# Performance work log

Measured on AMD Instinct MI355X. Metric: run time of the kernel, lower is better.

Reference implementation:

```python
import jax, jax.numpy as jnp
import numpy as np

DIM = 256          # model dim
HK = 8             # kv heads
HQ = 32            # query heads
H = HQ // HK       # queries per kv group
DH = 128           # head dim (== DIM//2, required by RoPE assert)
B = 1
T = 2048
THETA = 10000.0
CACHE = 8192       # RoPE cached seq_len; module uses _freqs_cis[-T:]


def _rope(x):
    # x: [..., T, DH]; positions are the LAST T of the cached 8192 (faithful to _freqs_cis[-T:])
    t = x.shape[-2]
    half = DH  # == DIM // 2
    pos = jnp.arange(CACHE - t, CACHE, dtype=jnp.float32)
    inv_freq = THETA ** (-(jnp.arange(half, dtype=jnp.float32) / half))
    f = pos[:, None] * inv_freq[None, :]            # [T, DH]
    cos, sin = jnp.cos(f), jnp.sin(f)
    x1, x2 = jnp.split(x, 2, axis=-1)
    rot = jnp.concatenate((-x2, x1), axis=-1)       # rotate_half
    return x * cos + rot * sin


def setup_inputs() -> dict:
    key = jax.random.key(0)
    ks = jax.random.split(key, 7)
    q = jax.random.normal(ks[0], (B, T, DIM), jnp.float32)
    k = jax.random.normal(ks[1], (B, T, DIM), jnp.float32)
    v = jax.random.normal(ks[2], (B, T, DIM), jnp.float32)
    mask = jnp.tril(jnp.ones((T, T), dtype=bool))   # causal
    Wq = jax.random.normal(ks[3], (DIM, HQ * DH), jnp.float32) * 0.02
    Wk = jax.random.normal(ks[4], (DIM, HK * DH), jnp.float32) * 0.02
    Wv = jax.random.normal(ks[5], (DIM, HK * DH), jnp.float32) * 0.02
    Wo = jax.random.normal(ks[6], (HQ * DH, DIM), jnp.float32) * 0.02
    return {"q": q, "k": k, "v": v, "mask": mask, "Wq": Wq, "Wk": Wk, "Wv": Wv, "Wo": Wo}


def reference(q, k, v, mask, Wq, Wk, Wv, Wo):
    b, t, _ = q.shape
    # projections + head split; query heads grouped as (HK, H)
    qi = (q @ Wq).reshape(b, t, HQ, DH).transpose(0, 2, 1, 3).reshape(b, HK, H, t, DH)
    ki = (k @ Wk).reshape(b, t, HK, DH).transpose(0, 2, 1, 3)  # [b, HK, t, DH]
    vi = (v @ Wv).reshape(b, t, HK, DH).transpose(0, 2, 1, 3)  # [b, HK, t, DH]
    # RoPE on q, k AND v (module applies _apply_rope to all three)
    qi = _rope(qi)
    ki = _rope(ki)
    vi = _rope(vi)
    s = jnp.einsum('bghid,bgjd->bghij', qi, ki) / jnp.sqrt(jnp.asarray(DH, qi.dtype))
    neg = -jnp.finfo(s.dtype).max
    s = jnp.where(mask, s, neg)
    attn = jax.nn.softmax(s, axis=-1)               # [b, HK, H, t, t]
    vals = jnp.einsum('bghij,bgjd->bghid', attn, vi)
    vals = vals.transpose(0, 3, 1, 2, 4).reshape(b, t, HQ * DH)
    return vals @ Wo
```

## Files before the change

### kernel.cpp

```cpp
#include <hip/hip_runtime.h>
#include <hip/hip_bf16.h>
#include <math.h>

#define TSEQ 2048
#define NHQ 32
#define NHK 8
#define DH 128

typedef __attribute__((ext_vector_type(8))) short short8;
typedef __attribute__((ext_vector_type(4))) float f32x4;
typedef __attribute__((ext_vector_type(4))) short s16x4;

__device__ __forceinline__ short f2bf(float f) {
  union { float f; unsigned u; } v; v.f = f;
  unsigned r = v.u + 0x7fffu + ((v.u >> 16) & 1u);
  return (short)(r >> 16);
}

__device__ __forceinline__ f32x4 zero4() {
  f32x4 z; z[0] = 0.f; z[1] = 0.f; z[2] = 0.f; z[3] = 0.f; return z;
}

__device__ __forceinline__ void async_cp16(const short* g, short* l) {
  __builtin_amdgcn_global_load_lds(
      (const __attribute__((address_space(1))) unsigned int*)g,
      (__attribute__((address_space(3))) unsigned int*)l, 16, 0, 0);
}

__global__ __launch_bounds__(256) void prep_transpose_kernel(
    const float* __restrict__ q, const float* __restrict__ k,
    const float* __restrict__ v, short* __restrict__ qkv,
    float* __restrict__ cosT, float* __restrict__ sinT,
    const float* __restrict__ Wq, const float* __restrict__ Wk,
    const float* __restrict__ Wv, const float* __restrict__ Wo,
    short* __restrict__ WqT, short* __restrict__ WkT,
    short* __restrict__ WvT, short* __restrict__ WoT) {
  __shared__ short tl[64][65];
  int bx = blockIdx.x, tid = threadIdx.x;
  if (bx < 1792) {
    int gid = bx * 256 + tid;
    if (gid < 393216) {
      int i4 = gid * 4;
      const float* src = (i4 < 524288) ? (q + i4)
                       : (i4 < 1048576 ? (k + i4 - 524288) : (v + i4 - 1048576));
      float f0 = src[0], f1 = src[1], f2 = src[2], f3 = src[3];
      s16x4 o; o[0] = f2bf(f0); o[1] = f2bf(f1); o[2] = f2bf(f2); o[3] = f2bf(f3);
      *(s16x4*)&qkv[i4] = o;
    } else if (gid < 458752) {
      int idx = (gid - 393216) * 4;
      int t = idx >> 7, d0 = idx & 127;
      float pos = (float)(8192 - TSEQ + t);
#pragma unroll
      for (int jj = 0; jj < 4; ++jj) {
        int d = d0 + jj;
        float inv = exp2f(-0.10381025296522977f * (float)d);
        float f = pos * inv;
        cosT[t * 128 + d] = cosf(f);
        sinT[t * 128 + d] = sinf(f);
      }
    }
    return;
  }
  int b = bx - 1792;
  const float* S; short* D; int K, N, tr, tc;
  if (b < 256)      { S = Wq; D = WqT; K = 256;  N = 4096; tr = b >> 6;        tc = b & 63; }
  else if (b < 320) { S = Wk; D = WkT; K = 256;  N = 1024; int t = b - 256; tr = t >> 4; tc = t & 15; }
  else if (b < 384) { S = Wv; D = WvT; K = 256;  N = 1024; int t = b - 320; tr = t >> 4; tc = t & 15; }
  else              { S = Wo; D = WoT; K = 4096; N = 256;  int t = b - 384; tr = t >> 2; tc = t & 3; }
  int k0 = tr * 64, n0 = tc * 64;
#pragma unroll
  for (int it = 0; it < 4; ++it) {
    int r = it * 16 + (tid >> 4), c = (tid & 15) * 4;
    const float* s = &S[(size_t)(k0 + r) * N + n0 + c];
    tl[r][c + 0] = f2bf(s[0]); tl[r][c + 1] = f2bf(s[1]);
    tl[r][c + 2] = f2bf(s[2]); tl[r][c + 3] = f2bf(s[3]);
  }
  __syncthreads();
#pragma unroll
  for (int it = 0; it < 4; ++it) {
    int rr = it * 16 + (tid >> 4), cc = (tid & 15) * 4;
    s16x4 o;
    o[0] = tl[cc + 0][rr]; o[1] = tl[cc + 1][rr];
    o[2] = tl[cc + 2][rr]; o[3] = tl[cc + 3][rr];
    *(s16x4*)&D[(size_t)(n0 + rr) * K + k0 + cc] = o;
  }
}

#define SCALE 0.08838834764831845f

__global__ __launch_bounds__(256) void proj_kernel(
    const short* __restrict__ qkv,
    const short* __restrict__ WqT, const short* __restrict__ WkT,
    const short* __restrict__ WvT,
    const float* __restrict__ cosT, const float* __restrict__ sinT,
    short* __restrict__ Qr, short* __restrict__ Kr, short* __restrict__ Vt) {
  __shared__ __attribute__((aligned(16))) short As[2][64 * 64];
  __shared__ __attribute__((aligned(16))) short Bs[2][128 * 64];
  int tid = threadIdx.x, lane = tid & 63, w = tid >> 6;
  int i = lane & 15, grp = lane >> 4;
  int bh = blockIdx.y, r0 = blockIdx.x * 64;
  const short* X; const short* Wt; short* dst; int vmode = 0;
  float oscale = 1.0f;
  if (bh < 32)      { X = qkv;                Wt = WqT + bh * (128 * 256);        dst = Qr + (size_t)bh * TSEQ * DH; oscale = SCALE; }
  else if (bh < 40) { X = qkv + TSEQ * 256;   Wt = WkT + (bh - 32) * (128 * 256); dst = Kr + (size_t)(bh - 32) * TSEQ * DH; }
  else              { X = qkv + 2 * TSEQ * 256; Wt = WvT + (bh - 40) * (128 * 256); dst = Vt + (size_t)(bh - 40) * DH * TSEQ; vmode = 1; }

  const short* srcA[2];
#pragma unroll
  for (int j = 0; j < 2; ++j) {
    int ci = w * 128 + j * 64 + lane;
    int row = ci >> 3, c = ci & 7;
    srcA[j] = X + (size_t)(r0 + row) * 256 + ((c ^ (row & 7)) << 3);
  }
  const short* srcB[4];
#pragma unroll
  for (int j = 0; j < 4; ++j) {
    int ci = w * 256 + j * 64 + lane;
    int row = ci >> 3, c = ci & 7;
    srcB[j] = Wt + (size_t)row * 256 + ((c ^ (row & 7)) << 3);
  }
  auto stage = [&](int kc_, int bsel) {
#pragma unroll
    for (int j = 0; j < 2; ++j)
      async_cp16(srcA[j] + kc_ * 64, &As[bsel][(w * 128 + j * 64) * 8]);
#pragma unroll
    for (int j = 0; j < 4; ++j)
      async_cp16(srcB[j] + kc_ * 64, &Bs[bsel][(w * 256 + j * 64) * 8]);
  };

  f32x4 acc[8];
#pragma unroll
  for (int n = 0; n < 8; ++n) acc[n] = zero4();

  stage(0, 0);
  for (int kc = 0; kc < 4; ++kc) {
    int buf = kc & 1;
    if (kc < 3) {
      stage(kc + 1, buf ^ 1);
      asm volatile("s_waitcnt vmcnt(6)" ::: "memory");
    } else {
      asm volatile("s_waitcnt vmcnt(0)" ::: "memory");
    }
    __builtin_amdgcn_s_barrier();
#pragma unroll
    for (int kc2 = 0; kc2 < 2; ++kc2) {
      short8 a = *(const short8*)&As[buf][(w * 16 + i) * 64 + (((kc2 * 4 + grp) ^ (i & 7)) * 8)];
#pragma unroll
      for (int n = 0; n < 8; ++n) {
        short8 bf = *(const short8*)&Bs[buf][(n * 16 + i) * 64 + (((kc2 * 4 + grp) ^ (i & 7)) * 8)];
        acc[n] = __builtin_amdgcn_mfma_f32_16x16x32_bf16(a, bf, acc[n], 0, 0, 0);
      }
    }
    __builtin_amdgcn_s_barrier();
  }
#pragma unroll
  for (int r = 0; r < 4; ++r) {
    int t = r0 + w * 16 + grp * 4 + r;
    const float* cr = cosT + (size_t)t * 128;
    const float* sr = sinT + (size_t)t * 128;
#pragma unroll
    for (int n = 0; n < 8; ++n) {
      int d = n * 16 + i;
      float x = acc[n][r];
      float xp = acc[n ^ 4][r];
      float rot = (n < 4) ? -xp : xp;
      float val = (x * cr[d] + rot * sr[d]) * oscale;
      short bv = f2bf(val);
      if (vmode) dst[(size_t)d * TSEQ + t] = bv;
      else       dst[(size_t)t * DH + d] = bv;
    }
  }
}

__global__ __launch_bounds__(512, 2) void attn_kernel(
    const short* __restrict__ Qr, const short* __restrict__ Kr,
    const short* __restrict__ Vt, short* __restrict__ Oa) {
  __shared__ __attribute__((aligned(16))) short Ks[2][64 * 128];
  __shared__ __attribute__((aligned(16))) short Vs[2][128 * 64];
  __shared__ __attribute__((aligned(16))) short Ps[8][16 * 72];
  int tid = threadIdx.x, lane = tid & 63, w = tid >> 6;
  int i = lane & 15, grp = lane >> 4;
  int b = blockIdx.x;
  int hk = b & 7, hq = (b >> 3) & 3, pr = b >> 5;
  int h = hk * 4 + hq;
  const short* Qh = Qr + (size_t)h * TSEQ * DH;
  const short* Kh = Kr + (size_t)hk * TSEQ * DH;
  const short* Vh = Vt + (size_t)hk * DH * TSEQ;

  const short* kst[2]; const short* vst[2];
#pragma unroll
  for (int hf = 0; hf < 2; ++hf) {
    int ci = hf * 512 + w * 64 + lane;
    int rk = ci >> 4, ck = ci & 15;
    kst[hf] = Kh + (size_t)rk * DH + ((ck ^ (rk & 15)) << 3);
    int rv = ci >> 3, cv = ci & 7;
    vst[hf] = Vh + (size_t)rv * TSEQ + ((cv ^ (rv & 7)) << 3);
  }

  for (int half = 0; half < 2; ++half) {
    int qt = half ? pr : (15 - pr);
    int q0 = qt * 128;
    int qq = q0 + w * 16 + i;
    short8 qf[4];
#pragma unroll
    for (int c = 0; c < 4; ++c)
      qf[c] = *(const short8*)&Qh[(size_t)qq * DH + c * 32 + grp * 8];

    f32x4 oacc[8];
#pragma unroll
    for (int n = 0; n < 8; ++n) oacc[n] = zero4();
    float mrow = -3.0e38f, lsum = 0.0f;

    int nt = 2 * qt + 2;
    int wave_max_row = q0 + w * 16 + 15;

    auto stage = [&](int kt_, int bsel) {
      int kv0_ = kt_ * 64;
      async_cp16(kst[0] + (size_t)kv0_ * DH, &Ks[bsel][w * 512]);
      async_cp16(kst[1] + (size_t)kv0_ * DH, &Ks[bsel][4096 + w * 512]);
      async_cp16(vst[0] + kv0_, &Vs[bsel][w * 512]);
      async_cp16(vst[1] + kv0_, &Vs[bsel][4096 + w * 512]);
    };

    stage(0, 0);
    for (int kt = 0; kt < nt; ++kt) {
      int kv0 = kt * 64;
      int buf = kt & 1;
      if (kt + 1 < nt) {
        stage(kt + 1, buf ^ 1);
        asm volatile("s_waitcnt vmcnt(4)" ::: "memory");
      } else {
        asm volatile("s_waitcnt vmcnt(0)" ::: "memory");
      }
      __builtin_amdgcn_s_barrier();
      if (kv0 <= wave_max_row) {
        const short* Kb = &Ks[buf][0];
        const short* Vb = &Vs[buf][0];
        f32x4 sacc[4];
#pragma unroll
        for (int n = 0; n < 4; ++n) sacc[n] = zero4();
        __builtin_amdgcn_s_setprio(1);
#pragma unroll
        for (int c = 0; c < 4; ++c) {
#pragma unroll
          for (int n = 0; n < 4; ++n) {
            short8 kb = *(const short8*)&Kb[(n * 16 + i) * 128 + (((c * 4 + grp) ^ i) * 8)];
            sacc[n] = __builtin_amdgcn_mfma_f32_16x16x32_bf16(kb, qf[c], sacc[n], 0, 0, 0);
          }
        }
        __builtin_amdgcn_s_setprio(0);
        bool diag = (kt >= nt - 2);
        float p_[4][4];
#pragma unroll
        for (int n = 0; n < 4; ++n)
#pragma unroll
          for (int r = 0; r < 4; ++r) {
            float s = sacc[n][r];
            if (diag) {
              int kk = kv0 + n * 16 + grp * 4 + r;
              if (kk > qq) s = -3.0e38f;
            }
            p_[n][r] = s;
          }
        float mnew = p_[0][0];
#pragma unroll
        for (int n = 0; n < 4; ++n)
#pragma unroll
          for (int r = 0; r < 4; ++r) mnew = fmaxf(mnew, p_[n][r]);
        mnew = fmaxf(mnew, __shfl_xor(mnew, 16));
        mnew = fmaxf(mnew, __shfl_xor(mnew, 32));
        if (__any((mnew > mrow + 8.0f) ? 1 : 0)) {
          float mn = fmaxf(mrow, mnew);
          float sfv = __expf(mrow - mn);
          mrow = mn;
          lsum *= sfv;
          float sf0 = __shfl(sfv, grp * 4 + 0);
          float sf1 = __shfl(sfv, grp * 4 + 1);
          float sf2 = __shfl(sfv, grp * 4 + 2);
          float sf3 = __shfl(sfv, grp * 4 + 3);
#pragma unroll
          for (int n = 0; n < 8; ++n) {
            oacc[n][0] *= sf0; oacc[n][1] *= sf1;
            oacc[n][2] *= sf2; oacc[n][3] *= sf3;
          }
        }
#pragma unroll
        for (int n = 0; n < 4; ++n) {
          float e0 = __expf(p_[n][0] - mrow);
          float e1 = __expf(p_[n][1] - mrow);
          float e2 = __expf(p_[n][2] - mrow);
          float e3 = __expf(p_[n][3] - mrow);
          lsum += (e0 + e1) + (e2 + e3);
          unsigned lo, hi;
          asm("v_cvt_pk_bf16_f32 %0, %1, %2" : "=v"(lo) : "v"(e0), "v"(e1));
          asm("v_cvt_pk_bf16_f32 %0, %1, %2" : "=v"(hi) : "v"(e2), "v"(e3));
          *(unsigned long long*)&Ps[w][i * 72 + n * 16 + grp * 4] =
              ((unsigned long long)hi << 32) | lo;
        }
        __builtin_amdgcn_s_setprio(1);
#pragma unroll
        for (int kc = 0; kc < 2; ++kc) {
          short8 pa = *(const short8*)&Ps[w][i * 72 + kc * 32 + grp * 8];
#pragma unroll
          for (int n = 0; n < 8; ++n) {
            short8 vb = *(const short8*)&Vb[(n * 16 + i) * 64 + (((kc * 4 + grp) ^ (i & 7)) * 8)];
            oacc[n] = __builtin_amdgcn_mfma_f32_16x16x32_bf16(pa, vb, oacc[n], 0, 0, 0);
          }
        }
        __builtin_amdgcn_s_setprio(0);
      }
      __builtin_amdgcn_s_barrier();
    }
    lsum += __shfl_xor(lsum, 16);
    lsum += __shfl_xor(lsum, 32);
    float inv[4];
#pragma unroll
    for (int r = 0; r < 4; ++r) inv[r] = 1.0f / __shfl(lsum, grp * 4 + r);
#pragma unroll
    for (int r = 0; r < 4; ++r) {
      int t = q0 + w * 16 + grp * 4 + r;
#pragma unroll
      for (int n = 0; n < 8; ++n) {
        int d = n * 16 + i;
        Oa[(size_t)t * 4096 + h * 128 + d] = f2bf(oacc[n][r] * inv[r]);
      }
    }
  }
}

__global__ __launch_bounds__(256) void outproj_kernel(
    const short* __restrict__ Oa, const short* __restrict__ WoT,
    float* __restrict__ Opart) {
  __shared__ __attribute__((aligned(16))) short As[2][128 * 64];
  __shared__ __attribute__((aligned(16))) short Bs[2][64 * 64];
  int tid = threadIdx.x, lane = tid & 63, w = tid >> 6;
  int i = lane & 15, grp = lane >> 4;
  int m0 = blockIdx.x * 128, n0 = blockIdx.y * 64, z = blockIdx.z;

  const short* srcA[4];
#pragma unroll
  for (int j = 0; j < 4; ++j) {
    int ci = w * 256 + j * 64 + lane;
    int row = ci >> 3, c = ci & 7;
    srcA[j] = Oa + (size_t)(m0 + row) * 4096 + (size_t)z * 1024 + ((c ^ (row & 7)) << 3);
  }
  const short* srcB[2];
#pragma unroll
  for (int j = 0; j < 2; ++j) {
    int ci = w * 128 + j * 64 + lane;
    int row = ci >> 3, c = ci & 7;
    srcB[j] = WoT + (size_t)(n0 + row) * 4096 + (size_t)z * 1024 + ((c ^ (row & 7)) << 3);
  }
  auto stage = [&](int kc_, int bsel) {
#pragma unroll
    for (int j = 0; j < 4; ++j)
      async_cp16(srcA[j] + kc_ * 64, &As[bsel][(w * 256 + j * 64) * 8]);
#pragma unroll
    for (int j = 0; j < 2; ++j)
      async_cp16(srcB[j] + kc_ * 64, &Bs[bsel][(w * 128 + j * 64) * 8]);
  };

  f32x4 acc[2][4];
#pragma unroll
  for (int mf = 0; mf < 2; ++mf)
#pragma unroll
    for (int nf = 0; nf < 4; ++nf) acc[mf][nf] = zero4();

  stage(0, 0);
  for (int kc = 0; kc < 16; ++kc) {
    int buf = kc & 1;
    if (kc < 15) {
      stage(kc + 1, buf ^ 1);
      asm volatile("s_waitcnt vmcnt(6)" ::: "memory");
    } else {
      asm volatile("s_waitcnt vmcnt(0)" ::: "memory");
    }
    __builtin_amdgcn_s_barrier();
#pragma unroll
    for (int kc2 = 0; kc2 < 2; ++kc2) {
#pragma unroll
      for (int mf = 0; mf < 2; ++mf) {
        short8 a = *(const short8*)&As[buf][(w * 32 + mf * 16 + i) * 64 + (((kc2 * 4 + grp) ^ (i & 7)) * 8)];
#pragma unroll
        for (int nf = 0; nf < 4; ++nf) {
          short8 bb = *(const short8*)&Bs[buf][(nf * 16 + i) * 64 + (((kc2 * 4 + grp) ^ (i & 7)) * 8)];
          acc[mf][nf] = __builtin_amdgcn_mfma_f32_16x16x32_bf16(a, bb, acc[mf][nf], 0, 0, 0);
        }
      }
    }
    __builtin_amdgcn_s_barrier();
  }
  float* dst = Opart + (size_t)z * (TSEQ * 256);
#pragma unroll
  for (int mf = 0; mf < 2; ++mf)
#pragma unroll
    for (int r = 0; r < 4; ++r) {
      int t = m0 + w * 32 + mf * 16 + grp * 4 + r;
#pragma unroll
      for (int nf = 0; nf < 4; ++nf)
        dst[(size_t)t * 256 + n0 + nf * 16 + i] = acc[mf][nf][r];
    }
}

__global__ __launch_bounds__(256) void reduce_kernel(
    const float* __restrict__ Opart, float* __restrict__ out) {
  int gid = blockIdx.x * 256 + threadIdx.x;
  int i4 = gid * 4;
  f32x4 s = *(const f32x4*)&Opart[i4];
#pragma unroll
  for (int z = 1; z < 4; ++z) {
    f32x4 p = *(const f32x4*)&Opart[(size_t)z * (TSEQ * 256) + i4];
    s[0] += p[0]; s[1] += p[1]; s[2] += p[2]; s[3] += p[3];
  }
  *(f32x4*)&out[i4] = s;
}

extern "C" void kernel_launch(void* const* d_in, const int* in_sizes, int n_in,
                              void* d_out, int out_size, void* d_ws, size_t ws_size,
                              hipStream_t stream) {
  const float* q  = (const float*)d_in[0];
  const float* k  = (const float*)d_in[1];
  const float* v  = (const float*)d_in[2];
  const float* Wq = (const float*)d_in[4];
  const float* Wk = (const float*)d_in[5];
  const float* Wv = (const float*)d_in[6];
  const float* Wo = (const float*)d_in[7];
  float* out = (float*)d_out;

  char* p = (char*)d_ws;
  auto take = [&](size_t nbytes) {
    char* r = p; p += (nbytes + 255) & ~(size_t)255; return r;
  };
  short* qkv  = (short*)take(3ull * TSEQ * 256 * 2);
  short* WqT  = (short*)take(4096ull * 256 * 2);
  short* WkT  = (short*)take(1024ull * 256 * 2);
  short* WvT  = (short*)take(1024ull * 256 * 2);
  short* WoT  = (short*)take(256ull * 4096 * 2);
  float* cosT = (float*)take((size_t)TSEQ * 128 * 4);
  float* sinT = (float*)take((size_t)TSEQ * 128 * 4);
  short* Qr   = (short*)take((size_t)NHQ * TSEQ * DH * 2);
  short* Kr   = (short*)take((size_t)NHK * TSEQ * DH * 2);
  short* Vt   = (short*)take((size_t)NHK * TSEQ * DH * 2);
  short* Oa   = (short*)take((size_t)TSEQ * 4096 * 2);
  float* Opart = (float*)Qr;

  hipLaunchKernelGGL(prep_transpose_kernel, dim3(2432), dim3(256), 0, stream,
                     q, k, v, qkv, cosT, sinT,
                     Wq, Wk, Wv, Wo, WqT, WkT, WvT, WoT);
  hipLaunchKernelGGL(proj_kernel, dim3(32, 48), dim3(256), 0, stream,
                     qkv, WqT, WkT, WvT, cosT, sinT, Qr, Kr, Vt);
  hipLaunchKernelGGL(attn_kernel, dim3(256), dim3(512), 0, stream,
                     Qr, Kr, Vt, Oa);
  hipLaunchKernelGGL(outproj_kernel, dim3(16, 4, 4), dim3(256), 0, stream,
                     Oa, WoT, Opart);
  hipLaunchKernelGGL(reduce_kernel, dim3(512), dim3(256), 0, stream,
                     Opart, out);
}
```

Measured before the change: 200.3 us.

## Drop LDS K/V staging; each wave handles 32 query rows with direct global loads

The attention kernel no longer double-buffers K and V tiles through shared memory with block-wide barriers. Each wave now loads K and V fragments straight from global memory, relying on the cache, and processes two 16-row query groups so every fragment feeds twice as many MFMAs. Waves 0-3 take one query tile and waves 4-7 its causal mirror, each stopping at its own causal bound. This removes barriers and LDS traffic, at the cost of exposed global-load latency, redundant K/V fetches across waves, and higher register pressure.

```diff
diff --git a/kernel.cpp b/kernel.cpp
--- a/kernel.cpp
+++ b/kernel.cpp
@@ -175,155 +175,153 @@
 __global__ __launch_bounds__(512, 2) void attn_kernel(
     const short* __restrict__ Qr, const short* __restrict__ Kr,
     const short* __restrict__ Vt, short* __restrict__ Oa) {
-  __shared__ __attribute__((aligned(16))) short Ks[2][64 * 128];
-  __shared__ __attribute__((aligned(16))) short Vs[2][128 * 64];
-  __shared__ __attribute__((aligned(16))) short Ps[8][16 * 72];
+  __shared__ __attribute__((aligned(16))) short Ps[8][32 * 72];
   int tid = threadIdx.x, lane = tid & 63, w = tid >> 6;
   int i = lane & 15, grp = lane >> 4;
   int b = blockIdx.x;
-  int hk = b & 7, hq = (b >> 3) & 3, pr = b >> 5;
+  int hk = b & 7, rr_ = b >> 3, qp = rr_ & 7, hq = rr_ >> 3;
   int h = hk * 4 + hq;
+  int qt = (w < 4) ? qp : (15 - qp);
+  int q0 = qt * 128 + (w & 3) * 32;
   const short* Qh = Qr + (size_t)h * TSEQ * DH;
   const short* Kh = Kr + (size_t)hk * TSEQ * DH;
   const short* Vh = Vt + (size_t)hk * DH * TSEQ;
-
-  const short* kst[2]; const short* vst[2];
-#pragma unroll
-  for (int hf = 0; hf < 2; ++hf) {
-    int ci = hf * 512 + w * 64 + lane;
-    int rk = ci >> 4, ck = ci & 15;
-    kst[hf] = Kh + (size_t)rk * DH + ((ck ^ (rk & 15)) << 3);
-    int rv = ci >> 3, cv = ci & 7;
-    vst[hf] = Vh + (size_t)rv * TSEQ + ((cv ^ (rv & 7)) << 3);
-  }
-
-  for (int half = 0; half < 2; ++half) {
-    int qt = half ? pr : (15 - pr);
-    int q0 = qt * 128;
-    int qq = q0 + w * 16 + i;
-    short8 qf[4];
+  short* Psw = &Ps[w][0];
+
+  short8 qf[2][4];
+#pragma unroll
+  for (int qr = 0; qr < 2; ++qr)
 #pragma unroll
     for (int c = 0; c < 4; ++c)
-      qf[c] = *(const short8*)&Qh[(size_t)qq * DH + c * 32 + grp * 8];
-
-    f32x4 oacc[8];
-#pragma unroll
-    for (int n = 0; n < 8; ++n) oacc[n] = zero4();
-    float mrow = -3.0e38f, lsum = 0.0f;
-
-    int nt = 2 * qt + 2;
-    int wave_max_row = q0 + w * 16 + 15;
-
-    auto stage = [&](int kt_, int bsel) {
-      int kv0_ = kt_ * 64;
-      async_cp16(kst[0] + (size_t)kv0_ * DH, &Ks[bsel][w * 512]);
-      async_cp16(kst[1] + (size_t)kv0_ * DH, &Ks[bsel][4096 + w * 512]);
-      async_cp16(vst[0] + kv0_, &Vs[bsel][w * 512]);
-      async_cp16(vst[1] + kv0_, &Vs[bsel][4096 + w * 512]);
-    };
-
-    stage(0, 0);
-    for (int kt = 0; kt < nt; ++kt) {
-      int kv0 = kt * 64;
-      int buf = kt & 1;
-      if (kt + 1 < nt) {
-        stage(kt + 1, buf ^ 1);
-        asm volatile("s_waitcnt vmcnt(4)" ::: "memory");
-      } else {
-        asm volatile("s_waitcnt vmcnt(0)" ::: "memory");
-      }
-      __builtin_amdgcn_s_barrier();
-      if (kv0 <= wave_max_row) {
-        const short* Kb = &Ks[buf][0];
-        const short* Vb = &Vs[buf][0];
-        f32x4 sacc[4];
-#pragma unroll
-        for (int n = 0; n < 4; ++n) sacc[n] = zero4();
-        __builtin_amdgcn_s_setprio(1);
-#pragma unroll
-        for (int c = 0; c < 4; ++c) {
-#pragma unroll
-          for (int n = 0; n < 4; ++n) {
-            short8 kb = *(const short8*)&Kb[(n * 16 + i) * 128 + (((c * 4 + grp) ^ i) * 8)];
-            sacc[n] = __builtin_amdgcn_mfma_f32_16x16x32_bf16(kb, qf[c], sacc[n], 0, 0, 0);
+      qf[qr][c] = *(const short8*)&Qh[(size_t)(q0 + qr * 16 + i) * DH + c * 32 + grp * 8];
+
+  f32x4 oacc[2][8];
+#pragma unroll
+  for (int qr = 0; qr < 2; ++qr)
+#pragma unroll
+    for (int n = 0; n < 8; ++n) oacc[qr][n] = zero4();
+  float mr0 = -3.0e38f, mr1 = -3.0e38f, ls0 = 0.f, ls1 = 0.f;
+
+  int nt = ((q0 + 31) >> 6) + 1;
+  for (int kt = 0; kt < nt; ++kt) {
+    int kv0 = kt * 64;
+    const short* Kt = Kh + (size_t)kv0 * DH;
+    f32x4 sacc[2][4];
+#pragma unroll
+    for (int qr = 0; qr < 2; ++qr)
+#pragma unroll
+      for (int n = 0; n < 4; ++n) sacc[qr][n] = zero4();
+    short8 kb0[4], kb1[4];
+#pragma unroll
+    for (int n = 0; n < 4; ++n)
+      kb0[n] = *(const short8*)&Kt[(size_t)(n * 16 + i) * DH + grp * 8];
+#pragma unroll
+    for (int c = 0; c < 4; ++c) {
+      if (c < 3) {
+#pragma unroll
+        for (int n = 0; n < 4; ++n)
+          kb1[n] = *(const short8*)&Kt[(size_t)(n * 16 + i) * DH + (c + 1) * 32 + grp * 8];
+      }
+#pragma unroll
+      for (int n = 0; n < 4; ++n) {
+        sacc[0][n] = __builtin_amdgcn_mfma_f32_16x16x32_bf16(kb0[n], qf[0][c], sacc[0][n], 0, 0, 0);
+        sacc[1][n] = __builtin_amdgcn_mfma_f32_16x16x32_bf16(kb0[n], qf[1][c], sacc[1][n], 0, 0, 0);
+      }
+#pragma unroll
+      for (int n = 0; n < 4; ++n) kb0[n] = kb1[n];
+    }
+    short8 vb0[8];
+#pragma unroll
+    for (int n = 0; n < 8; ++n)
+      vb0[n] = *(const short8*)&Vh[(size_t)(n * 16 + i) * TSEQ + kv0 + grp * 8];
+    if (kt == nt - 1) {
+#pragma unroll
+      for (int qr = 0; qr < 2; ++qr) {
+        int qq = q0 + qr * 16 + i;
+#pragma unroll
+        for (int n = 0; n < 4; ++n)
+#pragma unroll
+          for (int r = 0; r < 4; ++r) {
+            int kk = kv0 + n * 16 + grp * 4 + r;
+            if (kk > qq) sacc[qr][n][r] = -3.0e38f;
           }
-        }
-        __builtin_amdgcn_s_setprio(0);
-        bool diag = (kt >= nt - 2);
-        float p_[4][4];
-#pragma unroll
-        for (int n = 0; n < 4; ++n)
-#pragma unroll
-          for (int r = 0; r < 4; ++r) {
-            float s = sacc[n][r];
-            if (diag) {
-              int kk = kv0 + n * 16 + grp * 4 + r;
-              if (kk > qq) s = -3.0e38f;
-            }
-            p_[n][r] = s;
-          }
-        float mnew = p_[0][0];
-#pragma unroll
-        for (int n = 0; n < 4; ++n)
-#pragma unroll
-          for (int r = 0; r < 4; ++r) mnew = fmaxf(mnew, p_[n][r]);
-        mnew = fmaxf(mnew, __shfl_xor(mnew, 16));
-        mnew = fmaxf(mnew, __shfl_xor(mnew, 32));
-        if (__any((mnew > mrow + 8.0f) ? 1 : 0)) {
-          float mn = fmaxf(mrow, mnew);
-          float sfv = __expf(mrow - mn);
-          mrow = mn;
-          lsum *= sfv;
-          float sf0 = __shfl(sfv, grp * 4 + 0);
-          float sf1 = __shfl(sfv, grp * 4 + 1);
-          float sf2 = __shfl(sfv, grp * 4 + 2);
-          float sf3 = __shfl(sfv, grp * 4 + 3);
-#pragma unroll
-          for (int n = 0; n < 8; ++n) {
-            oacc[n][0] *= sf0; oacc[n][1] *= sf1;
-            oacc[n][2] *= sf2; oacc[n][3] *= sf3;
-          }
-        }
-#pragma unroll
-        for (int n = 0; n < 4; ++n) {
-          float e0 = __expf(p_[n][0] - mrow);
-          float e1 = __expf(p_[n][1] - mrow);
-          float e2 = __expf(p_[n][2] - mrow);
-          float e3 = __expf(p_[n][3] - mrow);
-          lsum += (e0 + e1) + (e2 + e3);
-          unsigned lo, hi;
-          asm("v_cvt_pk_bf16_f32 %0, %1, %2" : "=v"(lo) : "v"(e0), "v"(e1));
-          asm("v_cvt_pk_bf16_f32 %0, %1, %2" : "=v"(hi) : "v"(e2), "v"(e3));
-          *(unsigned long long*)&Ps[w][i * 72 + n * 16 + grp * 4] =
-              ((unsigned long long)hi << 32) | lo;
-        }
-        __builtin_amdgcn_s_setprio(1);
-#pragma unroll
-        for (int kc = 0; kc < 2; ++kc) {
-          short8 pa = *(const short8*)&Ps[w][i * 72 + kc * 32 + grp * 8];
-#pragma unroll
-          for (int n = 0; n < 8; ++n) {
-            short8 vb = *(const short8*)&Vb[(n * 16 + i) * 64 + (((kc * 4 + grp) ^ (i & 7)) * 8)];
-            oacc[n] = __builtin_amdgcn_mfma_f32_16x16x32_bf16(pa, vb, oacc[n], 0, 0, 0);
-          }
-        }
-        __builtin_amdgcn_s_setprio(0);
-      }
-      __builtin_amdgcn_s_barrier();
-    }
-    lsum += __shfl_xor(lsum, 16);
-    lsum += __shfl_xor(lsum, 32);
-    float inv[4];
-#pragma unroll
-    for (int r = 0; r < 4; ++r) inv[r] = 1.0f / __shfl(lsum, grp * 4 + r);
-#pragma unroll
-    for (int r = 0; r < 4; ++r) {
-      int t = q0 + w * 16 + grp * 4 + r;
+      }
+    }
+    float mn0 = sacc[0][0][0], mn1 = sacc[1][0][0];
+#pragma unroll
+    for (int n = 0; n < 4; ++n)
+#pragma unroll
+      for (int r = 0; r < 4; ++r) {
+        mn0 = fmaxf(mn0, sacc[0][n][r]);
+        mn1 = fmaxf(mn1, sacc[1][n][r]);
+      }
+    mn0 = fmaxf(mn0, __shfl_xor(mn0, 16)); mn0 = fmaxf(mn0, __shfl_xor(mn0, 32));
+    mn1 = fmaxf(mn1, __shfl_xor(mn1, 16)); mn1 = fmaxf(mn1, __shfl_xor(mn1, 32));
+    if (__any(((mn0 > mr0 + 8.0f) || (mn1 > mr1 + 8.0f)) ? 1 : 0)) {
+      float mx0 = fmaxf(mr0, mn0), mx1 = fmaxf(mr1, mn1);
+      float sf0 = __expf(mr0 - mx0), sf1 = __expf(mr1 - mx1);
+      mr0 = mx0; mr1 = mx1; ls0 *= sf0; ls1 *= sf1;
+#pragma unroll
+      for (int r = 0; r < 4; ++r) {
+        float f0 = __shfl(sf0, grp * 4 + r);
+        float f1 = __shfl(sf1, grp * 4 + r);
+#pragma unroll
+        for (int n = 0; n < 8; ++n) { oacc[0][n][r] *= f0; oacc[1][n][r] *= f1; }
+      }
+    }
+#pragma unroll
+    for (int qr = 0; qr < 2; ++qr) {
+      float mm = qr ? mr1 : mr0;
+      float lsv = 0.f;
+#pragma unroll
+      for (int n = 0; n < 4; ++n) {
+        float e0 = __expf(sacc[qr][n][0] - mm);
+        float e1 = __expf(sacc[qr][n][1] - mm);
+        float e2 = __expf(sacc[qr][n][2] - mm);
+        float e3 = __expf(sacc[qr][n][3] - mm);
+        lsv += (e0 + e1) + (e2 + e3);
+        unsigned lo, hi;
+        asm("v_cvt_pk_bf16_f32 %0, %1, %2" : "=v"(lo) : "v"(e0), "v"(e1));
+        asm("v_cvt_pk_bf16_f32 %0, %1, %2" : "=v"(hi) : "v"(e2), "v"(e3));
+        *(unsigned long long*)&Psw[(qr * 16 + i) * 72 + n * 16 + grp * 4] =
+            ((unsigned long long)hi << 32) | lo;
+      }
+      if (qr) ls1 += lsv; else ls0 += lsv;
+    }
+    short8 vb1[8];
+#pragma unroll
+    for (int n = 0; n < 8; ++n)
+      vb1[n] = *(const short8*)&Vh[(size_t)(n * 16 + i) * TSEQ + kv0 + 32 + grp * 8];
+    {
+      short8 pa0 = *(const short8*)&Psw[(0 * 16 + i) * 72 + grp * 8];
+      short8 pa1 = *(const short8*)&Psw[(1 * 16 + i) * 72 + grp * 8];
 #pragma unroll
       for (int n = 0; n < 8; ++n) {
-        int d = n * 16 + i;
-        Oa[(size_t)t * 4096 + h * 128 + d] = f2bf(oacc[n][r] * inv[r]);
-      }
+        oacc[0][n] = __builtin_amdgcn_mfma_f32_16x16x32_bf16(pa0, vb0[n], oacc[0][n], 0, 0, 0);
+        oacc[1][n] = __builtin_amdgcn_mfma_f32_16x16x32_bf16(pa1, vb0[n], oacc[1][n], 0, 0, 0);
+      }
+      pa0 = *(const short8*)&Psw[(0 * 16 + i) * 72 + 32 + grp * 8];
+      pa1 = *(const short8*)&Psw[(1 * 16 + i) * 72 + 32 + grp * 8];
+#pragma unroll
+      for (int n = 0; n < 8; ++n) {
+        oacc[0][n] = __builtin_amdgcn_mfma_f32_16x16x32_bf16(pa0, vb1[n], oacc[0][n], 0, 0, 0);
+        oacc[1][n] = __builtin_amdgcn_mfma_f32_16x16x32_bf16(pa1, vb1[n], oacc[1][n], 0, 0, 0);
+      }
+    }
+  }
+  ls0 += __shfl_xor(ls0, 16); ls0 += __shfl_xor(ls0, 32);
+  ls1 += __shfl_xor(ls1, 16); ls1 += __shfl_xor(ls1, 32);
+  float iv0 = 1.0f / ls0, iv1 = 1.0f / ls1;
+#pragma unroll
+  for (int r = 0; r < 4; ++r) {
+    float v0 = __shfl(iv0, grp * 4 + r);
+    float v1 = __shfl(iv1, grp * 4 + r);
+    int t0 = q0 + grp * 4 + r, t1 = q0 + 16 + grp * 4 + r;
+#pragma unroll
+    for (int n = 0; n < 8; ++n) {
+      int d = h * 128 + n * 16 + i;
+      Oa[(size_t)t0 * 4096 + d] = f2bf(oacc[0][n][r] * v0);
+      Oa[(size_t)t1 * 4096 + d] = f2bf(oacc[1][n][r] * v1);
     }
   }
 }
```

Measured after the change: 251.7 us. 1.26x slower.

## Split attention blocks per query tile, swizzle P tile, atomically reduce outproj

Applied to the files above, without the earlier changes.

Attention now launches one block per 128-row query tile (512 blocks) instead of pairing a long and a short tile per block, ordered heaviest first. This is meant to give more parallelism and finer load balancing. The P staging buffer switches from padded rows to an XOR-swizzled layout to avoid LDS bank conflicts. The split-K output projection now uses atomicAdd into a memset output, removing the separate reduce kernel and its partial buffer, at the cost of atomic traffic and nondeterministic summation order.

```diff
diff --git a/kernel.cpp b/kernel.cpp
--- a/kernel.cpp
+++ b/kernel.cpp
@@ -177,15 +177,18 @@
     const short* __restrict__ Vt, short* __restrict__ Oa) {
   __shared__ __attribute__((aligned(16))) short Ks[2][64 * 128];
   __shared__ __attribute__((aligned(16))) short Vs[2][128 * 64];
-  __shared__ __attribute__((aligned(16))) short Ps[8][16 * 72];
+  __shared__ __attribute__((aligned(16))) short Ps[8][16 * 64];
   int tid = threadIdx.x, lane = tid & 63, w = tid >> 6;
   int i = lane & 15, grp = lane >> 4;
   int b = blockIdx.x;
-  int hk = b & 7, hq = (b >> 3) & 3, pr = b >> 5;
+  int hk = b & 7, t_ = b >> 3, hq = t_ & 3, qrank = t_ >> 2;
+  int qt = 15 - qrank;
   int h = hk * 4 + hq;
+  int q0 = qt * 128;
   const short* Qh = Qr + (size_t)h * TSEQ * DH;
   const short* Kh = Kr + (size_t)hk * TSEQ * DH;
   const short* Vh = Vt + (size_t)hk * DH * TSEQ;
+  short* Psw = &Ps[w][0];
 
   const short* kst[2]; const short* vst[2];
 #pragma unroll
@@ -197,140 +200,136 @@
     vst[hf] = Vh + (size_t)rv * TSEQ + ((cv ^ (rv & 7)) << 3);
   }
 
-  for (int half = 0; half < 2; ++half) {
-    int qt = half ? pr : (15 - pr);
-    int q0 = qt * 128;
-    int qq = q0 + w * 16 + i;
-    short8 qf[4];
-#pragma unroll
-    for (int c = 0; c < 4; ++c)
-      qf[c] = *(const short8*)&Qh[(size_t)qq * DH + c * 32 + grp * 8];
-
-    f32x4 oacc[8];
-#pragma unroll
-    for (int n = 0; n < 8; ++n) oacc[n] = zero4();
-    float mrow = -3.0e38f, lsum = 0.0f;
-
-    int nt = 2 * qt + 2;
-    int wave_max_row = q0 + w * 16 + 15;
-
-    auto stage = [&](int kt_, int bsel) {
-      int kv0_ = kt_ * 64;
-      async_cp16(kst[0] + (size_t)kv0_ * DH, &Ks[bsel][w * 512]);
-      async_cp16(kst[1] + (size_t)kv0_ * DH, &Ks[bsel][4096 + w * 512]);
-      async_cp16(vst[0] + kv0_, &Vs[bsel][w * 512]);
-      async_cp16(vst[1] + kv0_, &Vs[bsel][4096 + w * 512]);
-    };
-
-    stage(0, 0);
-    for (int kt = 0; kt < nt; ++kt) {
-      int kv0 = kt * 64;
-      int buf = kt & 1;
-      if (kt + 1 < nt) {
-        stage(kt + 1, buf ^ 1);
-        asm volatile("s_waitcnt vmcnt(4)" ::: "memory");
-      } else {
-        asm volatile("s_waitcnt vmcnt(0)" ::: "memory");
-      }
-      __builtin_amdgcn_s_barrier();
-      if (kv0 <= wave_max_row) {
-        const short* Kb = &Ks[buf][0];
-        const short* Vb = &Vs[buf][0];
-        f32x4 sacc[4];
-#pragma unroll
-        for (int n = 0; n < 4; ++n) sacc[n] = zero4();
-        __builtin_amdgcn_s_setprio(1);
-#pragma unroll
-        for (int c = 0; c < 4; ++c) {
-#pragma unroll
-          for (int n = 0; n < 4; ++n) {
-            short8 kb = *(const short8*)&Kb[(n * 16 + i) * 128 + (((c * 4 + grp) ^ i) * 8)];
-            sacc[n] = __builtin_amdgcn_mfma_f32_16x16x32_bf16(kb, qf[c], sacc[n], 0, 0, 0);
+  int qq = q0 + w * 16 + i;
+  short8 qf[4];
+#pragma unroll
+  for (int c = 0; c < 4; ++c)
+    qf[c] = *(const short8*)&Qh[(size_t)qq * DH + c * 32 + grp * 8];
+
+  f32x4 oacc[8];
+#pragma unroll
+  for (int n = 0; n < 8; ++n) oacc[n] = zero4();
+  float mrow = -3.0e38f, lsum = 0.0f;
+
+  int nt = 2 * qt + 2;
+  int wave_max_row = q0 + w * 16 + 15;
+
+  auto stage = [&](int kt_, int bsel) {
+    int kv0_ = kt_ * 64;
+    async_cp16(kst[0] + (size_t)kv0_ * DH, &Ks[bsel][w * 512]);
+    async_cp16(kst[1] + (size_t)kv0_ * DH, &Ks[bsel][4096 + w * 512]);
+    async_cp16(vst[0] + kv0_, &Vs[bsel][w * 512]);
+    async_cp16(vst[1] + kv0_, &Vs[bsel][4096 + w * 512]);
+  };
+
+  stage(0, 0);
+  for (int kt = 0; kt < nt; ++kt) {
+    int kv0 = kt * 64;
+    int buf = kt & 1;
+    if (kt + 1 < nt) {
+      stage(kt + 1, buf ^ 1);
+      asm volatile("s_waitcnt vmcnt(4)" ::: "memory");
+    } else {
+      asm volatile("s_waitcnt vmcnt(0)" ::: "memory");
+    }
+    __builtin_amdgcn_s_barrier();
+    if (kv0 <= wave_max_row) {
+      const short* Kb = &Ks[buf][0];
+      const short* Vb = &Vs[buf][0];
+      f32x4 sacc[4];
+#pragma unroll
+      for (int n = 0; n < 4; ++n) sacc[n] = zero4();
+      __builtin_amdgcn_s_setprio(1);
+#pragma unroll
+      for (int c = 0; c < 4; ++c) {
+#pragma unroll
+        for (int n = 0; n < 4; ++n) {
+          short8 kb = *(const short8*)&Kb[(n * 16 + i) * 128 + (((c * 4 + grp) ^ i) * 8)];
+          sacc[n] = __builtin_amdgcn_mfma_f32_16x16x32_bf16(kb, qf[c], sacc[n], 0, 0, 0);
+        }
+      }
+      __builtin_amdgcn_s_setprio(0);
+      bool diag = (kt >= nt - 2);
+      float p_[4][4];
+#pragma unroll
+      for (int n = 0; n < 4; ++n)
+#pragma unroll
+        for (int r = 0; r < 4; ++r) {
+          float s = sacc[n][r];
+          if (diag) {
+            int kk = kv0 + n * 16 + grp * 4 + r;
+            if (kk > qq) s = -3.0e38f;
           }
+          p_[n][r] = s;
         }
-        __builtin_amdgcn_s_setprio(0);
-        bool diag = (kt >= nt - 2);
-        float p_[4][4];
-#pragma unroll
-        for (int n = 0; n < 4; ++n)
-#pragma unroll
-          for (int r = 0; r < 4; ++r) {
-            float s = sacc[n][r];
-            if (diag) {
-              int kk = kv0 + n * 16 + grp * 4 + r;
-              if (kk > qq) s = -3.0e38f;
-            }
-            p_[n][r] = s;
-          }
-        float mnew = p_[0][0];
-#pragma unroll
-        for (int n = 0; n < 4; ++n)
-#pragma unroll
-          for (int r = 0; r < 4; ++r) mnew = fmaxf(mnew, p_[n][r]);
-        mnew = fmaxf(mnew, __shfl_xor(mnew, 16));
-        mnew = fmaxf(mnew, __shfl_xor(mnew, 32));
-        if (__any((mnew > mrow + 8.0f) ? 1 : 0)) {
-          float mn = fmaxf(mrow, mnew);
-          float sfv = __expf(mrow - mn);
-          mrow = mn;
-          lsum *= sfv;
-          float sf0 = __shfl(sfv, grp * 4 + 0);
-          float sf1 = __shfl(sfv, grp * 4 + 1);
-          float sf2 = __shfl(sfv, grp * 4 + 2);
-          float sf3 = __shfl(sfv, grp * 4 + 3);
-#pragma unroll
-          for (int n = 0; n < 8; ++n) {
-            oacc[n][0] *= sf0; oacc[n][1] *= sf1;
-            oacc[n][2] *= sf2; oacc[n][3] *= sf3;
-          }
+      float mnew = p_[0][0];
+#pragma unroll
+      for (int n = 0; n < 4; ++n)
+#pragma unroll
+        for (int r = 0; r < 4; ++r) mnew = fmaxf(mnew, p_[n][r]);
+      mnew = fmaxf(mnew, __shfl_xor(mnew, 16));
+      mnew = fmaxf(mnew, __shfl_xor(mnew, 32));
+      if (__any((mnew > mrow + 8.0f) ? 1 : 0)) {
+        float mn = fmaxf(mrow, mnew);
+        float sfv = __expf(mrow - mn);
+        mrow = mn;
+        lsum *= sfv;
+        float sf0 = __shfl(sfv, grp * 4 + 0);
+        float sf1 = __shfl(sfv, grp * 4 + 1);
+        float sf2 = __shfl(sfv, grp * 4 + 2);
+        float sf3 = __shfl(sfv, grp * 4 + 3);
+#pragma unroll
+        for (int n = 0; n < 8; ++n) {
+          oacc[n][0] *= sf0; oacc[n][1] *= sf1;
+          oacc[n][2] *= sf2; oacc[n][3] *= sf3;
         }
-#pragma unroll
-        for (int n = 0; n < 4; ++n) {
-          float e0 = __expf(p_[n][0] - mrow);
-          float e1 = __expf(p_[n][1] - mrow);
-          float e2 = __expf(p_[n][2] - mrow);
-          float e3 = __expf(p_[n][3] - mrow);
-          lsum += (e0 + e1) + (e2 + e3);
-          unsigned lo, hi;
-          asm("v_cvt_pk_bf16_f32 %0, %1, %2" : "=v"(lo) : "v"(e0), "v"(e1));
-          asm("v_cvt_pk_bf16_f32 %0, %1, %2" : "=v"(hi) : "v"(e2), "v"(e3));
-          *(unsigned long long*)&Ps[w][i * 72 + n * 16 + grp * 4] =
-              ((unsigned long long)hi << 32) | lo;
+      }
+#pragma unroll
+      for (int n = 0; n < 4; ++n) {
+        float e0 = __expf(p_[n][0] - mrow);
+        float e1 = __expf(p_[n][1] - mrow);
+        float e2 = __expf(p_[n][2] - mrow);
+        float e3 = __expf(p_[n][3] - mrow);
+        lsum += (e0 + e1) + (e2 + e3);
+        unsigned lo, hi;
+        asm("v_cvt_pk_bf16_f32 %0, %1, %2" : "=v"(lo) : "v"(e0), "v"(e1));
+        asm("v_cvt_pk_bf16_f32 %0, %1, %2" : "=v"(hi) : "v"(e2), "v"(e3));
+        *(unsigned long long*)&Psw[i * 64 + (((2 * n + (grp >> 1)) ^ (i & 7)) * 8) + (grp & 1) * 4] =
+            ((unsigned long long)hi << 32) | lo;
+      }
+      __builtin_amdgcn_s_setprio(1);
+#pragma unroll
+      for (int kc = 0; kc < 2; ++kc) {
+        short8 pa = *(const short8*)&Psw[i * 64 + (((kc * 4 + grp) ^ (i & 7)) * 8)];
+#pragma unroll
+        for (int n = 0; n < 8; ++n) {
+          short8 vb = *(const short8*)&Vb[(n * 16 + i) * 64 + (((kc * 4 + grp) ^ (i & 7)) * 8)];
+          oacc[n] = __builtin_amdgcn_mfma_f32_16x16x32_bf16(pa, vb, oacc[n], 0, 0, 0);
         }
-        __builtin_amdgcn_s_setprio(1);
-#pragma unroll
-        for (int kc = 0; kc < 2; ++kc) {
-          short8 pa = *(const short8*)&Ps[w][i * 72 + kc * 32 + grp * 8];
-#pragma unroll
-          for (int n = 0; n < 8; ++n) {
-            short8 vb = *(const short8*)&Vb[(n * 16 + i) * 64 + (((kc * 4 + grp) ^ (i & 7)) * 8)];
-            oacc[n] = __builtin_amdgcn_mfma_f32_16x16x32_bf16(pa, vb, oacc[n], 0, 0, 0);
-          }
-        }
-        __builtin_amdgcn_s_setprio(0);
-      }
-      __builtin_amdgcn_s_barrier();
-    }
-    lsum += __shfl_xor(lsum, 16);
-    lsum += __shfl_xor(lsum, 32);
-    float inv[4];
-#pragma unroll
-    for (int r = 0; r < 4; ++r) inv[r] = 1.0f / __shfl(lsum, grp * 4 + r);
-#pragma unroll
-    for (int r = 0; r < 4; ++r) {
-      int t = q0 + w * 16 + grp * 4 + r;
-#pragma unroll
-      for (int n = 0; n < 8; ++n) {
-        int d = n * 16 + i;
-        Oa[(size_t)t * 4096 + h * 128 + d] = f2bf(oacc[n][r] * inv[r]);
-      }
+      }
+      __builtin_amdgcn_s_setprio(0);
+    }
+    __builtin_amdgcn_s_barrier();
+  }
+  lsum += __shfl_xor(lsum, 16);
+  lsum += __shfl_xor(lsum, 32);
+  float inv[4];
+#pragma unroll
+  for (int r = 0; r < 4; ++r) inv[r] = 1.0f / __shfl(lsum, grp * 4 + r);
+#pragma unroll
+  for (int r = 0; r < 4; ++r) {
+    int t = q0 + w * 16 + grp * 4 + r;
+#pragma unroll
+    for (int n = 0; n < 8; ++n) {
+      int d = n * 16 + i;
+      Oa[(size_t)t * 4096 + h * 128 + d] = f2bf(oacc[n][r] * inv[r]);
     }
   }
 }
 
 __global__ __launch_bounds__(256) void outproj_kernel(
     const short* __restrict__ Oa, const short* __restrict__ WoT,
-    float* __restrict__ Opart) {
+    float* __restrict__ out) {
   __shared__ __attribute__((aligned(16))) short As[2][128 * 64];
   __shared__ __attribute__((aligned(16))) short Bs[2][64 * 64];
   int tid = threadIdx.x, lane = tid & 63, w = tid >> 6;
@@ -390,7 +389,6 @@
     }
     __builtin_amdgcn_s_barrier();
   }
-  float* dst = Opart + (size_t)z * (TSEQ * 256);
 #pragma unroll
   for (int mf = 0; mf < 2; ++mf)
 #pragma unroll
@@ -398,21 +396,8 @@
       int t = m0 + w * 32 + mf * 16 + grp * 4 + r;
 #pragma unroll
       for (int nf = 0; nf < 4; ++nf)
-        dst[(size_t)t * 256 + n0 + nf * 16 + i] = acc[mf][nf][r];
-    }
-}
-
-__global__ __launch_bounds__(256) void reduce_kernel(
-    const float* __restrict__ Opart, float* __restrict__ out) {
-  int gid = blockIdx.x * 256 + threadIdx.x;
-  int i4 = gid * 4;
-  f32x4 s = *(const f32x4*)&Opart[i4];
-#pragma unroll
-  for (int z = 1; z < 4; ++z) {
-    f32x4 p = *(const f32x4*)&Opart[(size_t)z * (TSEQ * 256) + i4];
-    s[0] += p[0]; s[1] += p[1]; s[2] += p[2]; s[3] += p[3];
-  }
-  *(f32x4*)&out[i4] = s;
+        atomicAdd(&out[(size_t)t * 256 + n0 + nf * 16 + i], acc[mf][nf][r]);
+    }
 }
 
 extern "C" void kernel_launch(void* const* d_in, const int* in_sizes, int n_in,
@@ -442,17 +427,15 @@
   short* Kr   = (short*)take((size_t)NHK * TSEQ * DH * 2);
   short* Vt   = (short*)take((size_t)NHK * TSEQ * DH * 2);
   short* Oa   = (short*)take((size_t)TSEQ * 4096 * 2);
-  float* Opart = (float*)Qr;
-
+
+  hipMemsetAsync(out, 0, (size_t)out_size * sizeof(float), stream);
   hipLaunchKernelGGL(prep_transpose_kernel, dim3(2432), dim3(256), 0, stream,
                      q, k, v, qkv, cosT, sinT,
                      Wq, Wk, Wv, Wo, WqT, WkT, WvT, WoT);
   hipLaunchKernelGGL(proj_kernel, dim3(32, 48), dim3(256), 0, stream,
                      qkv, WqT, WkT, WvT, cosT, sinT, Qr, Kr, Vt);
-  hipLaunchKernelGGL(attn_kernel, dim3(256), dim3(512), 0, stream,
+  hipLaunchKernelGGL(attn_kernel, dim3(512), dim3(512), 0, stream,
                      Qr, Kr, Vt, Oa);
   hipLaunchKernelGGL(outproj_kernel, dim3(16, 4, 4), dim3(256), 0, stream,
-                     Oa, WoT, Opart);
-  hipLaunchKernelGGL(reduce_kernel, dim3(512), dim3(256), 0, stream,
-                     Opart, out);
-}
+                     Oa, WoT, out);
+}
```

Result: no change. 200.6 us (+0.1%).
